# Performance work log

Measured on AMD Instinct MI355X. Metric: run time of the kernel, lower is better.

Reference implementation:

```python
import jax, jax.numpy as jnp
import numpy as np

G, W, H1, H2, H3 = 512, 64, 128, 128, 64
B = 1024

def setup_inputs() -> dict:
    key = jax.random.key(0)
    k0, k1, k2, k3 = jax.random.split(key, 4)
    inputs = jax.random.normal(k0, (B, G * W), dtype=jnp.float32)
    # Glorot-uniform-like scaled init for stacked per-SKU weights
    def glorot(k, shape):
        fan_in, fan_out = shape[-2], shape[-1]
        lim = jnp.sqrt(6.0 / (fan_in + fan_out)).astype(jnp.float32)
        return jax.random.uniform(k, shape, jnp.float32, -lim, lim)
    W1 = glorot(k1, (G, W, H1))
    W2 = glorot(k2, (G, H1, H2))
    W3 = glorot(k3, (G, H2, H3))
    return {"inputs": inputs, "W1": W1, "W2": W2, "W3": W3}

def reference(inputs, W1, W2, W3):
    # inputs: [B, G*W]  -> per-SKU blocks [B, G, W] (SKU-major slicing in original)
    b = inputs.shape[0]
    x = inputs.reshape(b, G, W)
    # Grouped (batched-over-SKU) GEMM + relu per layer; no dropout (training=None)
    x = jax.nn.relu(jnp.einsum('bgw,gwh->bgh', x, W1))  # [B, G, H1]
    x = jax.nn.relu(jnp.einsum('bgh,ghk->bgk', x, W2))  # [B, G, H2]
    x = jax.nn.relu(jnp.einsum('bgk,gko->bgo', x, W3))  # [B, G, H3]
    # concat of per-SKU outputs along axis 1 == SKU-major reshape
    return x.reshape(b, G * H3)
```

## Files before the change

kernel.cpp:

```cpp
#include <hip/hip_runtime.h>

#define NG  512
#define GW  32768
#define GH3 32768

typedef __attribute__((ext_vector_type(8))) short bf16x8;
typedef __attribute__((ext_vector_type(4))) float f32x4;
typedef __attribute__((ext_vector_type(4))) unsigned int u32x4;
typedef __attribute__((ext_vector_type(2))) __bf16 bf16x2;

union frag_u { u32x4 u; bf16x8 h; };

#define MFMA __builtin_amdgcn_mfma_f32_16x16x32_bf16

__device__ __forceinline__ unsigned cvt2bf(float a, float b) {
  bf16x2 v = {(__bf16)a, (__bf16)b};
  return __builtin_bit_cast(unsigned, v);
}

__device__ __forceinline__ void permswap(unsigned &e, unsigned &o) {
  asm volatile("s_nop 1\n\t"
               "v_permlane32_swap_b32 %0, %1\n\t"
               "s_nop 1\n\t"
               "v_permlane16_swap_b32 %0, %1\n\t"
               "s_nop 1"
               : "+v"(e), "+v"(o));
}

__device__ __forceinline__ void mk_bfrag1(f32x4 e, f32x4 o, frag_u &bf) {
  unsigned E0 = cvt2bf(fmaxf(e[0], 0.f), fmaxf(e[1], 0.f));
  unsigned E1 = cvt2bf(fmaxf(e[2], 0.f), fmaxf(e[3], 0.f));
  unsigned O0 = cvt2bf(fmaxf(o[0], 0.f), fmaxf(o[1], 0.f));
  unsigned O1 = cvt2bf(fmaxf(o[2], 0.f), fmaxf(o[3], 0.f));
  permswap(E0, O0);
  permswap(E1, O1);
  bf.u = (u32x4){E0, E1, O0, O1};
}

template<int K, int H>
__device__ __forceinline__ void stage_frag(const float* __restrict__ gsrc,
                                           char* ldsBase, int tid) {
  constexpr int KC = K / 32;
  constexpr int NELEM = (K / 8) * H;
  #pragma unroll
  for (int lin = tid; lin < NELEM; lin += 512) {
    const int h  = lin & (H - 1);
    const int kb = lin / H;
    const float* p = gsrc + h + (size_t)(8 * kb) * H;
    unsigned w0 = cvt2bf(p[0 * H], p[1 * H]);
    unsigned w1 = cvt2bf(p[2 * H], p[3 * H]);
    unsigned w2 = cvt2bf(p[4 * H], p[5 * H]);
    unsigned w3 = cvt2bf(p[6 * H], p[7 * H]);
    const int mt = h >> 4, bl = h & 15, kc = kb >> 2, bq = kb & 3;
    const int byteoff = ((mt * KC + kc) * 64 + bq * 16 + bl) * 16;
    *(u32x4*)(ldsBase + byteoff) = (u32x4){w0, w1, w2, w3};
  }
}

__device__ __forceinline__ void ld_raw(const float* px, f32x4* d) {
  d[0] = *(const f32x4*)(px + 0);
  d[1] = *(const f32x4*)(px + 4);
  d[2] = *(const f32x4*)(px + 32);
  d[3] = *(const f32x4*)(px + 36);
}

__device__ __forceinline__ void cvt_b1(const f32x4* d, frag_u* b1) {
  b1[0].u = (u32x4){cvt2bf(d[0][0], d[0][1]), cvt2bf(d[0][2], d[0][3]),
                    cvt2bf(d[1][0], d[1][1]), cvt2bf(d[1][2], d[1][3])};
  b1[1].u = (u32x4){cvt2bf(d[2][0], d[2][1]), cvt2bf(d[2][2], d[2][3]),
                    cvt2bf(d[3][0], d[3][1]), cvt2bf(d[3][2], d[3][3])};
}

__global__ __launch_bounds__(512, 4)
void DeepBlockDense_kernel(const float* __restrict__ x,
                           const float* __restrict__ w1,
                           const float* __restrict__ w2,
                           const float* __restrict__ w3,
                           float* __restrict__ out) {
  __shared__ __align__(16) char smem[65536];
  const int g    = ((blockIdx.x & 7) << 6) + (blockIdx.x >> 3);
  const int tid  = threadIdx.x;
  const int lane = tid & 63;
  const int wid  = tid >> 6;
  const int bq   = lane >> 4;

  const float* xbase = x + g * 64 + 8 * bq + (size_t)(wid * 16 + (lane & 15)) * GW;

  f32x4 xra[4], xrb[4];
  ld_raw(xbase + (size_t)0   * GW, xra);
  ld_raw(xbase + (size_t)128 * GW, xrb);

  stage_frag<64 , 128>(w1 + (size_t)g * (64 * 128) , smem        , tid);
  stage_frag<128, 128>(w2 + (size_t)g * (128 * 128), smem + 16384, tid);
  stage_frag<128, 64 >(w3 + (size_t)g * (128 * 64) , smem + 49152, tid);
  __syncthreads();

  const char* aBase = smem + lane * 16;

  #pragma unroll 1
  for (int t = 0; t < 4; ++t) {
    const size_t r0 = (size_t)(t * 256 + wid * 16 + (lane & 15));
    const size_t r1 = r0 + 128;

    frag_u b1a[2], b1b[2];
    cvt_b1(xra, b1a);
    cvt_b1(xrb, b1b);
    if (t < 3) {
      ld_raw(xbase + (size_t)(t * 256 + 256) * GW, xra);
      ld_raw(xbase + (size_t)(t * 256 + 384) * GW, xrb);
    }

    frag_u b2a[4], b2b[4];
    #pragma unroll
    for (int pr = 0; pr < 4; ++pr) {
      f32x4 ea = {}, oa = {}, eb = {}, ob = {};
      #pragma unroll
      for (int kc = 0; kc < 2; ++kc) {
        frag_u ae, ao;
        ae.u = *(const u32x4*)(aBase + 1024 * ((2 * pr    ) * 2 + kc));
        ao.u = *(const u32x4*)(aBase + 1024 * ((2 * pr + 1) * 2 + kc));
        ea = MFMA(ae.h, b1a[kc].h, ea, 0, 0, 0);
        eb = MFMA(ae.h, b1b[kc].h, eb, 0, 0, 0);
        oa = MFMA(ao.h, b1a[kc].h, oa, 0, 0, 0);
        ob = MFMA(ao.h, b1b[kc].h, ob, 0, 0, 0);
      }
      mk_bfrag1(ea, oa, b2a[pr]);
      mk_bfrag1(eb, ob, b2b[pr]);
    }

    f32x4 acc3a[4] = {}, acc3b[4] = {};
    #pragma unroll
    for (int pr = 0; pr < 4; ++pr) {
      f32x4 ea = {}, oa = {}, eb = {}, ob = {};
      #pragma unroll
      for (int kc = 0; kc < 4; ++kc) {
        frag_u ae, ao;
        ae.u = *(const u32x4*)(aBase + 16384 + 1024 * ((2 * pr    ) * 4 + kc));
        ao.u = *(const u32x4*)(aBase + 16384 + 1024 * ((2 * pr + 1) * 4 + kc));
        ea = MFMA(ae.h, b2a[kc].h, ea, 0, 0, 0);
        eb = MFMA(ae.h, b2b[kc].h, eb, 0, 0, 0);
        oa = MFMA(ao.h, b2a[kc].h, oa, 0, 0, 0);
        ob = MFMA(ao.h, b2b[kc].h, ob, 0, 0, 0);
      }
      frag_u b3a, b3b;
      mk_bfrag1(ea, oa, b3a);
      mk_bfrag1(eb, ob, b3b);
      #pragma unroll
      for (int mt = 0; mt < 4; ++mt) {
        frag_u a;
        a.u = *(const u32x4*)(aBase + 49152 + 1024 * (mt * 4 + pr));
        acc3a[mt] = MFMA(a.h, b3a.h, acc3a[mt], 0, 0, 0);
        acc3b[mt] = MFMA(a.h, b3b.h, acc3b[mt], 0, 0, 0);
      }
    }

    float* po0 = out + r0 * GH3 + g * 64 + 4 * bq;
    float* po1 = out + r1 * GH3 + g * 64 + 4 * bq;
    #pragma unroll
    for (int mt = 0; mt < 4; ++mt) {
      f32x4 va = acc3a[mt];
      va[0] = fmaxf(va[0], 0.f); va[1] = fmaxf(va[1], 0.f);
      va[2] = fmaxf(va[2], 0.f); va[3] = fmaxf(va[3], 0.f);
      __builtin_nontemporal_store(va, (f32x4*)(po0 + 16 * mt));
    }
    #pragma unroll
    for (int mt = 0; mt < 4; ++mt) {
      f32x4 vb = acc3b[mt];
      vb[0] = fmaxf(vb[0], 0.f); vb[1] = fmaxf(vb[1], 0.f);
      vb[2] = fmaxf(vb[2], 0.f); vb[3] = fmaxf(vb[3], 0.f);
      __builtin_nontemporal_store(vb, (f32x4*)(po1 + 16 * mt));
    }
  }
}

extern "C" void kernel_launch(void* const* d_in, const int* in_sizes, int n_in,
                              void* d_out, int out_size, void* d_ws, size_t ws_size,
                              hipStream_t stream) {
  const float* x  = (const float*)d_in[0];
  const float* w1 = (const float*)d_in[1];
  const float* w2 = (const float*)d_in[2];
  const float* w3 = (const float*)d_in[3];
  float* out = (float*)d_out;
  (void)in_sizes; (void)n_in; (void)out_size; (void)d_ws; (void)ws_size;
  DeepBlockDense_kernel<<<dim3(NG), dim3(512), 0, stream>>>(x, w1, w2, w3, out);
}
```

Baseline: 70.98 us.

## Process two SKU groups per 1024-thread block with 128KB shared weights

Result: no change. 70.81 us (-0.3%).

```diff
diff --git a/kernel.cpp b/kernel.cpp
--- a/kernel.cpp
+++ b/kernel.cpp
@@ -71,43 +71,50 @@
                     cvt2bf(d[3][0], d[3][1]), cvt2bf(d[3][2], d[3][3])};
 }
 
-__global__ __launch_bounds__(512, 4)
+__global__ __launch_bounds__(1024, 4)
 void DeepBlockDense_kernel(const float* __restrict__ x,
                            const float* __restrict__ w1,
                            const float* __restrict__ w2,
                            const float* __restrict__ w3,
                            float* __restrict__ out) {
-  __shared__ __align__(16) char smem[65536];
-  const int g    = ((blockIdx.x & 7) << 6) + (blockIdx.x >> 3);
+  __shared__ __align__(16) char smem[131072];
+  const int gp   = ((blockIdx.x & 7) << 5) + (blockIdx.x >> 3);
+  const int g0   = gp * 2;
   const int tid  = threadIdx.x;
   const int lane = tid & 63;
   const int wid  = tid >> 6;
   const int bq   = lane >> 4;
 
-  const float* xbase = x + g * 64 + 8 * bq + (size_t)(wid * 16 + (lane & 15)) * GW;
-
+  const size_t row0 = (size_t)(wid * 16 + (lane & 15));
   f32x4 xra[4], xrb[4];
-  ld_raw(xbase + (size_t)0   * GW, xra);
-  ld_raw(xbase + (size_t)128 * GW, xrb);
-
-  stage_frag<64 , 128>(w1 + (size_t)g * (64 * 128) , smem        , tid);
-  stage_frag<128, 128>(w2 + (size_t)g * (128 * 128), smem + 16384, tid);
-  stage_frag<128, 64 >(w3 + (size_t)g * (128 * 64) , smem + 49152, tid);
+  ld_raw(x + row0 * GW + g0 * 64 +  0 + 8 * bq, xra);
+  ld_raw(x + row0 * GW + g0 * 64 + 64 + 8 * bq, xrb);
+
+  {
+    const int half = tid >> 9;
+    const int t512 = tid & 511;
+    char* base = smem + (half << 16);
+    const size_t gg = (size_t)(g0 + half);
+    stage_frag<64 , 128>(w1 + gg * (64 * 128) , base        , t512);
+    stage_frag<128, 128>(w2 + gg * (128 * 128), base + 16384, t512);
+    stage_frag<128, 64 >(w3 + gg * (128 * 64) , base + 49152, t512);
+  }
   __syncthreads();
 
-  const char* aBase = smem + lane * 16;
+  const char* aBase0 = smem + lane * 16;
+  const char* aBase1 = smem + 65536 + lane * 16;
 
   #pragma unroll 1
   for (int t = 0; t < 4; ++t) {
-    const size_t r0 = (size_t)(t * 256 + wid * 16 + (lane & 15));
-    const size_t r1 = r0 + 128;
+    const size_t r = (size_t)(t * 256 + wid * 16 + (lane & 15));
 
     frag_u b1a[2], b1b[2];
     cvt_b1(xra, b1a);
     cvt_b1(xrb, b1b);
     if (t < 3) {
-      ld_raw(xbase + (size_t)(t * 256 + 256) * GW, xra);
-      ld_raw(xbase + (size_t)(t * 256 + 384) * GW, xrb);
+      const size_t rn = r + 256;
+      ld_raw(x + rn * GW + g0 * 64 +  0 + 8 * bq, xra);
+      ld_raw(x + rn * GW + g0 * 64 + 64 + 8 * bq, xrb);
     }
 
     frag_u b2a[4], b2b[4];
@@ -116,13 +123,17 @@
       f32x4 ea = {}, oa = {}, eb = {}, ob = {};
       #pragma unroll
       for (int kc = 0; kc < 2; ++kc) {
-        frag_u ae, ao;
-        ae.u = *(const u32x4*)(aBase + 1024 * ((2 * pr    ) * 2 + kc));
-        ao.u = *(const u32x4*)(aBase + 1024 * ((2 * pr + 1) * 2 + kc));
-        ea = MFMA(ae.h, b1a[kc].h, ea, 0, 0, 0);
-        eb = MFMA(ae.h, b1b[kc].h, eb, 0, 0, 0);
-        oa = MFMA(ao.h, b1a[kc].h, oa, 0, 0, 0);
-        ob = MFMA(ao.h, b1b[kc].h, ob, 0, 0, 0);
+        const int oe = 1024 * ((2 * pr    ) * 2 + kc);
+        const int oo = 1024 * ((2 * pr + 1) * 2 + kc);
+        frag_u ae0, ao0, ae1, ao1;
+        ae0.u = *(const u32x4*)(aBase0 + oe);
+        ao0.u = *(const u32x4*)(aBase0 + oo);
+        ae1.u = *(const u32x4*)(aBase1 + oe);
+        ao1.u = *(const u32x4*)(aBase1 + oo);
+        ea = MFMA(ae0.h, b1a[kc].h, ea, 0, 0, 0);
+        eb = MFMA(ae1.h, b1b[kc].h, eb, 0, 0, 0);
+        oa = MFMA(ao0.h, b1a[kc].h, oa, 0, 0, 0);
+        ob = MFMA(ao1.h, b1b[kc].h, ob, 0, 0, 0);
       }
       mk_bfrag1(ea, oa, b2a[pr]);
       mk_bfrag1(eb, ob, b2b[pr]);
@@ -134,41 +145,46 @@
       f32x4 ea = {}, oa = {}, eb = {}, ob = {};
       #pragma unroll
       for (int kc = 0; kc < 4; ++kc) {
-        frag_u ae, ao;
-        ae.u = *(const u32x4*)(aBase + 16384 + 1024 * ((2 * pr    ) * 4 + kc));
-        ao.u = *(const u32x4*)(aBase + 16384 + 1024 * ((2 * pr + 1) * 4 + kc));
-        ea = MFMA(ae.h, b2a[kc].h, ea, 0, 0, 0);
-        eb = MFMA(ae.h, b2b[kc].h, eb, 0, 0, 0);
-        oa = MFMA(ao.h, b2a[kc].h, oa, 0, 0, 0);
-        ob = MFMA(ao.h, b2b[kc].h, ob, 0, 0, 0);
+        const int oe = 16384 + 1024 * ((2 * pr    ) * 4 + kc);
+        const int oo = 16384 + 1024 * ((2 * pr + 1) * 4 + kc);
+        frag_u ae0, ao0, ae1, ao1;
+        ae0.u = *(const u32x4*)(aBase0 + oe);
+        ao0.u = *(const u32x4*)(aBase0 + oo);
+        ae1.u = *(const u32x4*)(aBase1 + oe);
+        ao1.u = *(const u32x4*)(aBase1 + oo);
+        ea = MFMA(ae0.h, b2a[kc].h, ea, 0, 0, 0);
+        eb = MFMA(ae1.h, b2b[kc].h, eb, 0, 0, 0);
+        oa = MFMA(ao0.h, b2a[kc].h, oa, 0, 0, 0);
+        ob = MFMA(ao1.h, b2b[kc].h, ob, 0, 0, 0);
       }
       frag_u b3a, b3b;
       mk_bfrag1(ea, oa, b3a);
       mk_bfrag1(eb, ob, b3b);
       #pragma unroll
       for (int mt = 0; mt < 4; ++mt) {
-        frag_u a;
-        a.u = *(const u32x4*)(aBase + 49152 + 1024 * (mt * 4 + pr));
-        acc3a[mt] = MFMA(a.h, b3a.h, acc3a[mt], 0, 0, 0);
-        acc3b[mt] = MFMA(a.h, b3b.h, acc3b[mt], 0, 0, 0);
+        const int o3 = 49152 + 1024 * (mt * 4 + pr);
+        frag_u a0, a1;
+        a0.u = *(const u32x4*)(aBase0 + o3);
+        a1.u = *(const u32x4*)(aBase1 + o3);
+        acc3a[mt] = MFMA(a0.h, b3a.h, acc3a[mt], 0, 0, 0);
+        acc3b[mt] = MFMA(a1.h, b3b.h, acc3b[mt], 0, 0, 0);
       }
     }
 
-    float* po0 = out + r0 * GH3 + g * 64 + 4 * bq;
-    float* po1 = out + r1 * GH3 + g * 64 + 4 * bq;
+    float* po = out + r * GH3 + g0 * 64 + 4 * bq;
     #pragma unroll
     for (int mt = 0; mt < 4; ++mt) {
       f32x4 va = acc3a[mt];
       va[0] = fmaxf(va[0], 0.f); va[1] = fmaxf(va[1], 0.f);
       va[2] = fmaxf(va[2], 0.f); va[3] = fmaxf(va[3], 0.f);
-      __builtin_nontemporal_store(va, (f32x4*)(po0 + 16 * mt));
+      __builtin_nontemporal_store(va, (f32x4*)(po + 16 * mt));
     }
     #pragma unroll
     for (int mt = 0; mt < 4; ++mt) {
       f32x4 vb = acc3b[mt];
       vb[0] = fmaxf(vb[0], 0.f); vb[1] = fmaxf(vb[1], 0.f);
       vb[2] = fmaxf(vb[2], 0.f); vb[3] = fmaxf(vb[3], 0.f);
-      __builtin_nontemporal_store(vb, (f32x4*)(po1 + 16 * mt));
+      __builtin_nontemporal_store(vb, (f32x4*)(po + 64 + 16 * mt));
     }
   }
 }
@@ -182,5 +198,5 @@
   const float* w3 = (const float*)d_in[3];
   float* out = (float*)d_out;
   (void)in_sizes; (void)n_in; (void)out_size; (void)d_ws; (void)ws_size;
-  DeepBlockDense_kernel<<<dim3(NG), dim3(512), 0, stream>>>(x, w1, w2, w3, out);
-}
+  DeepBlockDense_kernel<<<dim3(NG / 2), dim3(1024), 0, stream>>>(x, w1, w2, w3, out);
+}
```
